# Kernel tuning notes

Hardware: AMD Instinct MI355X
Metric: run time of the kernel (lower is better)

Reference implementation:

```python
import jax, jax.numpy as jnp
import numpy as np

EPS = 1e-5  # torch BatchNorm2d default


def _signature_depth3(path):
    """Truncated (depth-3) path signature via Chen's relation.
    path: [B, P, ch] (P points). Returns [B, ch + ch^2 + ch^3] in signatory
    layout (level 1, then row-major flattened levels 2 and 3)."""
    dx = path[:, 1:] - path[:, :-1]  # [B, P-1, ch] increments
    B, _, ch = dx.shape

    def step(carry, v):
        s1, s2, s3 = carry  # [B,ch], [B,ch,ch], [B,ch,ch,ch]
        vv = v[:, :, None] * v[:, None, :]          # v (x) v
        e2 = 0.5 * vv                               # v^(x)2 / 2!
        e3 = vv[:, :, :, None] * v[:, None, None, :] / 6.0  # v^(x)3 / 3!
        n1 = s1 + v
        n2 = s2 + s1[:, :, None] * v[:, None, :] + e2
        n3 = (s3
              + s2[:, :, :, None] * v[:, None, None, :]
              + s1[:, :, None, None] * e2[:, None, :, :]
              + e3)
        return (n1, n2, n3), None

    init = (jnp.zeros((B, ch), dx.dtype),
            jnp.zeros((B, ch, ch), dx.dtype),
            jnp.zeros((B, ch, ch, ch), dx.dtype))
    (s1, s2, s3), _ = jax.lax.scan(step, init, jnp.transpose(dx, (1, 0, 2)))
    return jnp.concatenate([s1, s2.reshape(B, -1), s3.reshape(B, -1)], axis=1)


def setup_inputs() -> dict:
    key = jax.random.key(0)
    ks = jax.random.split(key, 5)
    N, C, J, T, L = 16, 64, 25, 128, 9
    sic, out_dim = 8, 64
    ch = sic + 1                      # +1 time channel
    sig_ch = ch + ch**2 + ch**3       # 819
    x = jax.random.normal(ks[0], (N, C, J, T, L), jnp.float32)
    conv_w = jax.random.normal(ks[1], (sic, C), jnp.float32) * 0.1
    conv_b = jax.random.normal(ks[2], (sic,), jnp.float32) * 0.1
    bn_gamma = jnp.ones((sic,), jnp.float32)
    bn_beta = jnp.zeros((sic,), jnp.float32)
    lin_w = jax.random.normal(ks[3], (out_dim, sig_ch), jnp.float32) * 0.03
    lin_b = jax.random.normal(ks[4], (out_dim,), jnp.float32) * 0.03
    return dict(x=x, conv_w=conv_w, conv_b=conv_b, bn_gamma=bn_gamma,
                bn_beta=bn_beta, lin_w=lin_w, lin_b=lin_b)


def reference(x, conv_w, conv_b, bn_gamma, bn_beta, lin_w, lin_b):
    N, C, J, T, L = x.shape
    # 1x1 conv over channel dim (applied to [N*L, C, J, T] in torch, which is
    # the same per-position linear map)
    y = jnp.einsum('ncjtl,oc->nojtl', x, conv_w) + conv_b[None, :, None, None, None]
    y = jax.nn.relu(y)
    # BatchNorm2d (training mode): stats over all dims except channel
    mean = y.mean(axis=(0, 2, 3, 4), keepdims=True)
    var = ((y - mean) ** 2).mean(axis=(0, 2, 3, 4), keepdims=True)
    y = ((y - mean) * jax.lax.rsqrt(var + EPS)
         * bn_gamma[None, :, None, None, None] + bn_beta[None, :, None, None, None])
    # -> [N*J*T, L, sic] stream per (n, joint, frame)
    B = N * J * T
    p = jnp.transpose(y, (0, 2, 3, 4, 1)).reshape(B, L, -1)
    # signatory.Augment(include_time=True): prepend time channel in [0, 1]
    t = jnp.broadcast_to(jnp.linspace(0.0, 1.0, L, dtype=x.dtype)[None, :, None], (B, L, 1))
    p = jnp.concatenate([t, p], axis=-1)  # [B, L, ch]
    # signature(..., basepoint=True): prepend zero point
    path = jnp.concatenate([jnp.zeros((B, 1, p.shape[-1]), p.dtype), p], axis=1)
    sig = _signature_depth3(path)          # [B, 819]
    z = sig @ lin_w.T + lin_b              # [B, out_dim]
    return jnp.transpose(z.reshape(N, J, T, -1), (0, 3, 1, 2))  # [N, C, J, T]
```

## Files before the change

kernel.cpp:

```cpp
#include <hip/hip_runtime.h>
#include <hip/hip_bf16.h>

typedef unsigned short u16;
typedef __attribute__((ext_vector_type(8))) short short8;
typedef __attribute__((ext_vector_type(4))) float f32x4;

#define N_    16
#define C_    64
#define J_    25
#define T_    128
#define L_    9
#define SIC   8
#define OUT_  64
#define BTOT  (N_*J_*T_)
#define CNT   (BTOT*L_)
#define KPAD  896
#define SPB   28

#define K1_BLOCKS 512
#define K1_ACT    225

#define PART_OFF  0
#define PART2_OFF 16384
#define SS_OFF    32768
#define BT_OFF    40960
#define Y_OFF     69632
#define WS_NEED   ((size_t)(Y_OFF + BTOT*72) * 4)

__device__ __forceinline__ short to_bf16(float x) {
  union { __hip_bfloat16 h; u16 u; } cv;
  cv.h = __float2bfloat16(x);
  return (short)cv.u;
}

__global__ __launch_bounds__(256) void k1_conv(
    const float* __restrict__ x, const float* __restrict__ cw,
    const float* __restrict__ cb, float* __restrict__ yws,
    float* __restrict__ part) {
  __shared__ float wl[SIC * C_];
  __shared__ float bl[SIC];
  __shared__ float wsum[4][16];
  int tid = threadIdx.x;
  wl[tid] = cw[tid];
  wl[tid + 256] = cw[tid + 256];
  if (tid < SIC) bl[tid] = cb[tid];
  __syncthreads();

  float vals[16];
#pragma unroll
  for (int q = 0; q < 16; q++) vals[q] = 0.f;

  if (tid < K1_ACT) {
    int p0 = (blockIdx.x * K1_ACT + tid) * 4;
    int n = p0 / 28800, rem = p0 % 28800;
    int jj = rem / 1152, tl0 = rem % 1152;
    const float* xp = x + (size_t)(n * 1600 + jj) * 1152 + tl0;

    float acc[4][8];
#pragma unroll
    for (int p = 0; p < 4; p++)
#pragma unroll
      for (int o = 0; o < 8; o++) acc[p][o] = bl[o];

#pragma unroll 8
    for (int c = 0; c < C_; c++) {
      float4 xv = *(const float4*)(xp + (size_t)c * 28800);
#pragma unroll
      for (int o = 0; o < 8; o++) {
        float wv = wl[o * C_ + c];
        acc[0][o] = fmaf(xv.x, wv, acc[0][o]);
        acc[1][o] = fmaf(xv.y, wv, acc[1][o]);
        acc[2][o] = fmaf(xv.z, wv, acc[2][o]);
        acc[3][o] = fmaf(xv.w, wv, acc[3][o]);
      }
    }
    float4* dst = (float4*)(yws + (size_t)p0 * 8);
#pragma unroll
    for (int p = 0; p < 4; p++) {
#pragma unroll
      for (int o = 0; o < 8; o++) acc[p][o] = fmaxf(acc[p][o], 0.f);
      dst[p * 2]     = make_float4(acc[p][0], acc[p][1], acc[p][2], acc[p][3]);
      dst[p * 2 + 1] = make_float4(acc[p][4], acc[p][5], acc[p][6], acc[p][7]);
#pragma unroll
      for (int o = 0; o < 8; o++) {
        vals[o] += acc[p][o];
        vals[8 + o] += acc[p][o] * acc[p][o];
      }
    }
  }

  int lane = tid & 63, wid = tid >> 6;
#pragma unroll
  for (int v = 0; v < 16; v++) {
    float s = vals[v];
    for (int off = 32; off > 0; off >>= 1) s += __shfl_down(s, off, 64);
    if (lane == 0) wsum[wid][v] = s;
  }
  __syncthreads();
  if (tid < 16)
    part[blockIdx.x * 16 + tid] = wsum[0][tid] + wsum[1][tid] + wsum[2][tid] + wsum[3][tid];
}

__global__ __launch_bounds__(256) void k2_red1(
    const float* __restrict__ part, float* __restrict__ part2) {
  __shared__ float red[16][16];
  int tid = threadIdx.x;
  int val = tid & 15, grp = tid >> 4;
  red[grp][val] = part[(blockIdx.x * 16 + grp) * 16 + val];
  __syncthreads();
  if (tid < 16) {
    float tot = 0.f;
#pragma unroll
    for (int g = 0; g < 16; g++) tot += red[g][tid];
    part2[blockIdx.x * 16 + tid] = tot;
  }
}

__global__ __launch_bounds__(256) void k2_stats2(
    const float* __restrict__ part2, const float* __restrict__ gamma,
    const float* __restrict__ beta, float* __restrict__ ss) {
  __shared__ float red[16][16];
  int tid = threadIdx.x;
  int val = tid & 15, grp = tid >> 4;
  red[grp][val] = part2[grp * 16 + val] + part2[(grp + 16) * 16 + val];
  __syncthreads();
  if (tid < 16) {
    float tot = 0.f;
#pragma unroll
    for (int g = 0; g < 16; g++) tot += red[g][tid];
    red[0][tid] = tot;
  }
  __syncthreads();
  if (tid < 8) {
    float mean = red[0][tid] * (1.f / CNT);
    float var  = red[0][8 + tid] * (1.f / CNT) - mean * mean;
    float sc = gamma[tid] * rsqrtf(var + 1e-5f);
    ss[tid] = sc;
    ss[8 + tid] = beta[tid] - mean * sc;
  }
}

__global__ __launch_bounds__(256) void k2_bt(
    const float* __restrict__ lw, u16* __restrict__ Bt) {
  int idx = blockIdx.x * 256 + threadIdx.x;
  if (idx >= OUT_ * KPAD) return;
  int o = idx / KPAD, k = idx % KPAD;
  float v = 0.f;
  if (k < 864) {
    int i = k / 96, p = k % 96;
    if (p < 91) {
      int orig = (p == 0) ? i : (p < 10 ? 9 + i * 9 + (p - 1) : 90 + i * 81 + (p - 10));
      v = lw[o * 819 + orig];
    }
  }
  Bt[idx] = (u16)to_bf16(v);
}

__global__ __launch_bounds__(256, 2) void k3_fused(
    const float* __restrict__ yws, const float* __restrict__ ss,
    const u16* __restrict__ Bt, const float* __restrict__ lb,
    float* __restrict__ out) {
  __shared__ __align__(16) u16 sig_lds[32 * KPAD];
  __shared__ __align__(16) float ylds[SPB * 72];
  __shared__ float ssl[16];
  __shared__ float lbl[64];
  int tid = threadIdx.x;
  if (tid < 16) ssl[tid] = ss[tid];
  if (tid >= 64 && tid < 128) lbl[tid - 64] = lb[tid - 64];
  int gBase = blockIdx.x * SPB;
  int valid = BTOT - gBase; if (valid > SPB) valid = SPB;
  __syncthreads();

  if (tid < SPB * 9) {
    int s = tid / 9;
    if (s < valid) {
      const float4* src = (const float4*)(yws + (size_t)gBase * 72 + (size_t)tid * 8);
      float4 a = src[0], b = src[1];
      float* drow = ylds + tid * 8;
      drow[0] = fmaf(a.x, ssl[0], ssl[8]);
      drow[1] = fmaf(a.y, ssl[1], ssl[9]);
      drow[2] = fmaf(a.z, ssl[2], ssl[10]);
      drow[3] = fmaf(a.w, ssl[3], ssl[11]);
      drow[4] = fmaf(b.x, ssl[4], ssl[12]);
      drow[5] = fmaf(b.y, ssl[5], ssl[13]);
      drow[6] = fmaf(b.z, ssl[6], ssl[14]);
      drow[7] = fmaf(b.w, ssl[7], ssl[15]);
    }
  }
  __syncthreads();

  int s = tid / 9, i = tid % 9;
  bool act = (tid < SPB * 9) && (s < valid);
  if (act) {
    const float* yrow = ylds + s * 72;
    int i1 = (i == 0) ? 0 : (i - 1);
    float s1 = 0.f, s2[9], s3[81], prev[8], prevvi = 0.f;
#pragma unroll
    for (int jj = 0; jj < 9; jj++) s2[jj] = 0.f;
#pragma unroll
    for (int q = 0; q < 81; q++) s3[q] = 0.f;
#pragma unroll
    for (int c = 0; c < 8; c++) prev[c] = 0.f;

#pragma unroll 3
    for (int l = 0; l < 9; l++) {
      float4 a4 = *(const float4*)(yrow + l * 8);
      float4 b4 = *(const float4*)(yrow + l * 8 + 4);
      float ldsv = yrow[l * 8 + i1];
      float cur[8] = {a4.x, a4.y, a4.z, a4.w, b4.x, b4.y, b4.z, b4.w};
      float v[9];
      v[0] = (l == 0) ? 0.f : 0.125f;
#pragma unroll
      for (int c = 0; c < 8; c++) v[c + 1] = cur[c] - prev[c];
      float curvi = (i == 0) ? (float)l * 0.125f : ldsv;
      float vi = curvi - prevvi;
      prevvi = curvi;
      float aa = fmaf(vi, (1.f / 6.f), 0.5f * s1);
      float b2 = fmaf(vi, 0.5f, s1);
#pragma unroll
      for (int jj = 0; jj < 9; jj++) {
        float tj = fmaf(aa, v[jj], s2[jj]);
#pragma unroll
        for (int k = 0; k < 9; k++) s3[jj * 9 + k] = fmaf(tj, v[k], s3[jj * 9 + k]);
        s2[jj] = fmaf(b2, v[jj], s2[jj]);
      }
      s1 += vi;
#pragma unroll
      for (int c = 0; c < 8; c++) prev[c] = cur[c];
    }

    u16* rowbase = sig_lds + s * KPAD;
    int sw = s & 7;
    {
      short8 ch;
      ch[0] = to_bf16(s1);
#pragma unroll
      for (int w = 0; w < 7; w++) ch[w + 1] = to_bf16(s2[w]);
      *(short8*)&rowbase[(((i * 12 + 0) ^ sw) * 8)] = ch;
    }
    {
      short8 ch;
      ch[0] = to_bf16(s2[7]); ch[1] = to_bf16(s2[8]);
#pragma unroll
      for (int w = 0; w < 6; w++) ch[w + 2] = to_bf16(s3[w]);
      *(short8*)&rowbase[(((i * 12 + 1) ^ sw) * 8)] = ch;
    }
#pragma unroll
    for (int c = 2; c <= 10; c++) {
      short8 ch;
#pragma unroll
      for (int w = 0; w < 8; w++) ch[w] = to_bf16(s3[c * 8 - 10 + w]);
      *(short8*)&rowbase[(((i * 12 + c) ^ sw) * 8)] = ch;
    }
    {
      short8 ch;
      ch[0] = to_bf16(s3[78]); ch[1] = to_bf16(s3[79]); ch[2] = to_bf16(s3[80]);
      ch[3] = 0; ch[4] = 0; ch[5] = 0; ch[6] = 0; ch[7] = 0;
      *(short8*)&rowbase[(((i * 12 + 11) ^ sw) * 8)] = ch;
    }
    if (i < 4) {
      short8 z = {0, 0, 0, 0, 0, 0, 0, 0};
      *(short8*)&rowbase[(((108 + i) ^ sw) * 8)] = z;
    }
  }
  {
    short8 z = {0, 0, 0, 0, 0, 0, 0, 0};
    int padChunks = (32 - valid) * 112;
    for (int e = tid; e < padChunks; e += 256) {
      int r = valid + e / 112, sl = e % 112;
      *(short8*)&sig_lds[r * KPAD + sl * 8] = z;
    }
  }
  __syncthreads();

  int w = tid >> 6, l = tid & 63;
  int brow = (w << 4) + (l & 15);
  const short8* bp = (const short8*)(Bt + (size_t)brow * KPAD);
  int arow0 = (l & 15), arow1 = 16 + (l & 15);
  int asw = arow0 & 7;
  f32x4 acc0 = {0, 0, 0, 0}, acc1 = {0, 0, 0, 0};
#pragma unroll
  for (int ks = 0; ks < 28; ks++) {
    int s4 = ks * 4 + (l >> 4);
    short8 bfrag = bp[s4];
    short8 a0 = *(const short8*)&sig_lds[arow0 * KPAD + ((s4 ^ asw) * 8)];
    short8 a1 = *(const short8*)&sig_lds[arow1 * KPAD + ((s4 ^ asw) * 8)];
    acc0 = __builtin_amdgcn_mfma_f32_16x16x32_bf16(a0, bfrag, acc0, 0, 0, 0);
    acc1 = __builtin_amdgcn_mfma_f32_16x16x32_bf16(a1, bfrag, acc1, 0, 0, 0);
  }
  __syncthreads();

  float* c_lds = (float*)sig_lds;
  int o = (w << 4) + (l & 15);
#pragma unroll
  for (int r = 0; r < 4; r++) {
    int m0 = (l >> 4) * 4 + r;
    c_lds[o * 33 + m0] = acc0[r];
    c_lds[o * 33 + 16 + m0] = acc1[r];
  }
  __syncthreads();
  for (int e = tid; e < 2048; e += 256) {
    int o2 = e >> 5, m = e & 31;
    if (m < valid) {
      int b = gBase + m;
      int n = b / (J_ * T_), rem = b % (J_ * T_);
      int j = rem >> 7, t = rem & (T_ - 1);
      out[(((size_t)n * OUT_ + o2) * J_ + j) * T_ + t] = c_lds[o2 * 33 + m] + lbl[o2];
    }
  }
}

extern "C" void kernel_launch(void* const* d_in, const int* in_sizes, int n_in,
                              void* d_out, int out_size, void* d_ws, size_t ws_size,
                              hipStream_t stream) {
  const float* x     = (const float*)d_in[0];
  const float* cw    = (const float*)d_in[1];
  const float* cb    = (const float*)d_in[2];
  const float* gamma = (const float*)d_in[3];
  const float* beta  = (const float*)d_in[4];
  const float* lw    = (const float*)d_in[5];
  const float* lbias = (const float*)d_in[6];
  float* out = (float*)d_out;
  float* ws  = (float*)d_ws;
  if (ws_size < WS_NEED) return;

  float* part  = ws + PART_OFF;
  float* part2 = ws + PART2_OFF;
  float* ss    = ws + SS_OFF;
  u16*   bt    = (u16*)(ws + BT_OFF);
  float* yws   = ws + Y_OFF;

  hipLaunchKernelGGL(k2_bt, dim3((OUT_ * KPAD + 255) / 256), dim3(256), 0, stream, lw, bt);
  hipLaunchKernelGGL(k1_conv, dim3(K1_BLOCKS), dim3(256), 0, stream, x, cw, cb, yws, part);
  hipLaunchKernelGGL(k2_red1, dim3(32), dim3(256), 0, stream, part, part2);
  hipLaunchKernelGGL(k2_stats2, dim3(1), dim3(256), 0, stream, part2, gamma, beta, ss);

  int nblk3 = (BTOT + SPB - 1) / SPB;
  hipLaunchKernelGGL(k3_fused, dim3(nblk3), dim3(256), 0, stream, yws, ss, bt, lbias, out);
}
```

Measured before the change: 81.46 us.

## Merge weight prep into conv, collapse stats reduction, shrink LDS for occupancy

Folds the bf16 weight-transposition kernel into the conv kernel as extra blocks and merges the two stat-reduction kernels into one, cutting the launch count from five to three. The conv kernel now gives each thread two positions instead of four and uses all 256 threads, with transposed weights in LDS so they load as vectors. The fused signature kernel aliases the normalized-input staging buffer onto the signature LDS tile, uses 29 rows instead of 32, and skips the last K step, allowing three blocks per CU. This adds an extra barrier before signature writes and clamps out-of-range MFMA rows, which increases register pressure under the new launch bound.

Measured after the change: 70.82 us. 13.1% less time.

```diff
diff --git a/kernel.cpp b/kernel.cpp
--- a/kernel.cpp
+++ b/kernel.cpp
@@ -15,16 +15,17 @@
 #define BTOT  (N_*J_*T_)
 #define CNT   (BTOT*L_)
 #define KPAD  896
+#define NKS   27
 #define SPB   28
 
-#define K1_BLOCKS 512
-#define K1_ACT    225
+#define K1C_BLOCKS 900
+#define K1BT_BLOCKS 224
+#define BT_ELEMS (OUT_*KPAD)
 
 #define PART_OFF  0
-#define PART2_OFF 16384
-#define SS_OFF    32768
-#define BT_OFF    40960
-#define Y_OFF     69632
+#define SS_OFF    16384
+#define BT_OFF    32768
+#define Y_OFF     65536
 #define WS_NEED   ((size_t)(Y_OFF + BTOT*72) * 4)
 
 __device__ __forceinline__ short to_bf16(float x) {
@@ -35,57 +36,75 @@
 
 __global__ __launch_bounds__(256) void k1_conv(
     const float* __restrict__ x, const float* __restrict__ cw,
-    const float* __restrict__ cb, float* __restrict__ yws,
-    float* __restrict__ part) {
-  __shared__ float wl[SIC * C_];
+    const float* __restrict__ cb, const float* __restrict__ lw,
+    float* __restrict__ yws, float* __restrict__ part, u16* __restrict__ Bt) {
+  int tid = threadIdx.x;
+
+  if (blockIdx.x >= K1C_BLOCKS) {
+    int idx = (blockIdx.x - K1C_BLOCKS) * 256 + tid;
+    if (idx < BT_ELEMS) {
+      int o = idx / KPAD, k = idx % KPAD;
+      float v = 0.f;
+      if (k < 864) {
+        int i = k / 96, p = k % 96;
+        if (p < 91) {
+          int orig = (p == 0) ? i : (p < 10 ? 9 + i * 9 + (p - 1) : 90 + i * 81 + (p - 10));
+          v = lw[o * 819 + orig];
+        }
+      }
+      Bt[idx] = (u16)to_bf16(v);
+    }
+    return;
+  }
+
+  __shared__ float wlT[C_ * SIC];
   __shared__ float bl[SIC];
   __shared__ float wsum[4][16];
-  int tid = threadIdx.x;
-  wl[tid] = cw[tid];
-  wl[tid + 256] = cw[tid + 256];
+  wlT[tid] = cw[(tid & 7) * C_ + (tid >> 3)];
+  wlT[tid + 256] = cw[(tid & 7) * C_ + ((tid + 256) >> 3)];
   if (tid < SIC) bl[tid] = cb[tid];
   __syncthreads();
 
+  int p0 = (blockIdx.x * 256 + tid) * 2;
+  int n = p0 / 28800, rem = p0 % 28800;
+  int jj = rem / 1152, tl0 = rem % 1152;
+  const float* xp = x + (size_t)(n * 1600 + jj) * 1152 + tl0;
+
+  float acc[2][8];
+#pragma unroll
+  for (int p = 0; p < 2; p++)
+#pragma unroll
+    for (int o = 0; o < 8; o++) acc[p][o] = bl[o];
+
+#pragma unroll 8
+  for (int c = 0; c < C_; c++) {
+    float2 xv = *(const float2*)(xp + (size_t)c * 28800);
+    float4 w0 = *(const float4*)&wlT[c * 8];
+    float4 w1 = *(const float4*)&wlT[c * 8 + 4];
+    acc[0][0] = fmaf(xv.x, w0.x, acc[0][0]); acc[1][0] = fmaf(xv.y, w0.x, acc[1][0]);
+    acc[0][1] = fmaf(xv.x, w0.y, acc[0][1]); acc[1][1] = fmaf(xv.y, w0.y, acc[1][1]);
+    acc[0][2] = fmaf(xv.x, w0.z, acc[0][2]); acc[1][2] = fmaf(xv.y, w0.z, acc[1][2]);
+    acc[0][3] = fmaf(xv.x, w0.w, acc[0][3]); acc[1][3] = fmaf(xv.y, w0.w, acc[1][3]);
+    acc[0][4] = fmaf(xv.x, w1.x, acc[0][4]); acc[1][4] = fmaf(xv.y, w1.x, acc[1][4]);
+    acc[0][5] = fmaf(xv.x, w1.y, acc[0][5]); acc[1][5] = fmaf(xv.y, w1.y, acc[1][5]);
+    acc[0][6] = fmaf(xv.x, w1.z, acc[0][6]); acc[1][6] = fmaf(xv.y, w1.z, acc[1][6]);
+    acc[0][7] = fmaf(xv.x, w1.w, acc[0][7]); acc[1][7] = fmaf(xv.y, w1.w, acc[1][7]);
+  }
+
   float vals[16];
 #pragma unroll
   for (int q = 0; q < 16; q++) vals[q] = 0.f;
-
-  if (tid < K1_ACT) {
-    int p0 = (blockIdx.x * K1_ACT + tid) * 4;
-    int n = p0 / 28800, rem = p0 % 28800;
-    int jj = rem / 1152, tl0 = rem % 1152;
-    const float* xp = x + (size_t)(n * 1600 + jj) * 1152 + tl0;
-
-    float acc[4][8];
-#pragma unroll
-    for (int p = 0; p < 4; p++)
-#pragma unroll
-      for (int o = 0; o < 8; o++) acc[p][o] = bl[o];
-
-#pragma unroll 8
-    for (int c = 0; c < C_; c++) {
-      float4 xv = *(const float4*)(xp + (size_t)c * 28800);
-#pragma unroll
-      for (int o = 0; o < 8; o++) {
-        float wv = wl[o * C_ + c];
-        acc[0][o] = fmaf(xv.x, wv, acc[0][o]);
-        acc[1][o] = fmaf(xv.y, wv, acc[1][o]);
-        acc[2][o] = fmaf(xv.z, wv, acc[2][o]);
-        acc[3][o] = fmaf(xv.w, wv, acc[3][o]);
-      }
-    }
-    float4* dst = (float4*)(yws + (size_t)p0 * 8);
-#pragma unroll
-    for (int p = 0; p < 4; p++) {
-#pragma unroll
-      for (int o = 0; o < 8; o++) acc[p][o] = fmaxf(acc[p][o], 0.f);
-      dst[p * 2]     = make_float4(acc[p][0], acc[p][1], acc[p][2], acc[p][3]);
-      dst[p * 2 + 1] = make_float4(acc[p][4], acc[p][5], acc[p][6], acc[p][7]);
-#pragma unroll
-      for (int o = 0; o < 8; o++) {
-        vals[o] += acc[p][o];
-        vals[8 + o] += acc[p][o] * acc[p][o];
-      }
+  float4* dst = (float4*)(yws + (size_t)p0 * 8);
+#pragma unroll
+  for (int p = 0; p < 2; p++) {
+#pragma unroll
+    for (int o = 0; o < 8; o++) acc[p][o] = fmaxf(acc[p][o], 0.f);
+    dst[p * 2]     = make_float4(acc[p][0], acc[p][1], acc[p][2], acc[p][3]);
+    dst[p * 2 + 1] = make_float4(acc[p][4], acc[p][5], acc[p][6], acc[p][7]);
+#pragma unroll
+    for (int o = 0; o < 8; o++) {
+      vals[o] += acc[p][o];
+      vals[8 + o] += acc[p][o] * acc[p][o];
     }
   }
 
@@ -101,28 +120,22 @@
     part[blockIdx.x * 16 + tid] = wsum[0][tid] + wsum[1][tid] + wsum[2][tid] + wsum[3][tid];
 }
 
-__global__ __launch_bounds__(256) void k2_red1(
-    const float* __restrict__ part, float* __restrict__ part2) {
-  __shared__ float red[16][16];
-  int tid = threadIdx.x;
-  int val = tid & 15, grp = tid >> 4;
-  red[grp][val] = part[(blockIdx.x * 16 + grp) * 16 + val];
-  __syncthreads();
-  if (tid < 16) {
-    float tot = 0.f;
-#pragma unroll
-    for (int g = 0; g < 16; g++) tot += red[g][tid];
-    part2[blockIdx.x * 16 + tid] = tot;
-  }
-}
-
-__global__ __launch_bounds__(256) void k2_stats2(
-    const float* __restrict__ part2, const float* __restrict__ gamma,
+__global__ __launch_bounds__(256) void k2_stats(
+    const float* __restrict__ part, const float* __restrict__ gamma,
     const float* __restrict__ beta, float* __restrict__ ss) {
   __shared__ float red[16][16];
   int tid = threadIdx.x;
   int val = tid & 15, grp = tid >> 4;
-  red[grp][val] = part2[grp * 16 + val] + part2[(grp + 16) * 16 + val];
+  float s0 = 0.f, s1 = 0.f, s2 = 0.f, s3 = 0.f;
+  int b = grp;
+  for (; b + 48 < K1C_BLOCKS; b += 64) {
+    s0 += part[b * 16 + val];
+    s1 += part[(b + 16) * 16 + val];
+    s2 += part[(b + 32) * 16 + val];
+    s3 += part[(b + 48) * 16 + val];
+  }
+  for (; b < K1C_BLOCKS; b += 16) s0 += part[b * 16 + val];
+  red[grp][val] = (s0 + s1) + (s2 + s3);
   __syncthreads();
   if (tid < 16) {
     float tot = 0.f;
@@ -140,30 +153,14 @@
   }
 }
 
-__global__ __launch_bounds__(256) void k2_bt(
-    const float* __restrict__ lw, u16* __restrict__ Bt) {
-  int idx = blockIdx.x * 256 + threadIdx.x;
-  if (idx >= OUT_ * KPAD) return;
-  int o = idx / KPAD, k = idx % KPAD;
-  float v = 0.f;
-  if (k < 864) {
-    int i = k / 96, p = k % 96;
-    if (p < 91) {
-      int orig = (p == 0) ? i : (p < 10 ? 9 + i * 9 + (p - 1) : 90 + i * 81 + (p - 10));
-      v = lw[o * 819 + orig];
-    }
-  }
-  Bt[idx] = (u16)to_bf16(v);
-}
-
-__global__ __launch_bounds__(256, 2) void k3_fused(
+__global__ __launch_bounds__(256, 3) void k3_fused(
     const float* __restrict__ yws, const float* __restrict__ ss,
     const u16* __restrict__ Bt, const float* __restrict__ lb,
     float* __restrict__ out) {
-  __shared__ __align__(16) u16 sig_lds[32 * KPAD];
-  __shared__ __align__(16) float ylds[SPB * 72];
+  __shared__ __align__(16) u16 sig_lds[29 * KPAD];
   __shared__ float ssl[16];
   __shared__ float lbl[64];
+  float* ylds = (float*)sig_lds;
   int tid = threadIdx.x;
   if (tid < 16) ssl[tid] = ss[tid];
   if (tid >= 64 && tid < 128) lbl[tid - 64] = lb[tid - 64];
@@ -187,18 +184,27 @@
       drow[7] = fmaf(b.w, ssl[7], ssl[15]);
     }
   }
+  {
+    short8 z = {0, 0, 0, 0, 0, 0, 0, 0};
+    int padChunks = (29 - valid) * 112;
+    for (int e = tid; e < padChunks; e += 256) {
+      int r = valid + e / 112, sl = e % 112;
+      *(short8*)&sig_lds[r * KPAD + sl * 8] = z;
+    }
+  }
   __syncthreads();
 
   int s = tid / 9, i = tid % 9;
   bool act = (tid < SPB * 9) && (s < valid);
+  float s1 = 0.f, s2[9], s3[81];
+#pragma unroll
+  for (int jj = 0; jj < 9; jj++) s2[jj] = 0.f;
+#pragma unroll
+  for (int q = 0; q < 81; q++) s3[q] = 0.f;
   if (act) {
     const float* yrow = ylds + s * 72;
     int i1 = (i == 0) ? 0 : (i - 1);
-    float s1 = 0.f, s2[9], s3[81], prev[8], prevvi = 0.f;
-#pragma unroll
-    for (int jj = 0; jj < 9; jj++) s2[jj] = 0.f;
-#pragma unroll
-    for (int q = 0; q < 81; q++) s3[q] = 0.f;
+    float prev[8], prevvi = 0.f;
 #pragma unroll
     for (int c = 0; c < 8; c++) prev[c] = 0.f;
 
@@ -228,7 +234,10 @@
 #pragma unroll
       for (int c = 0; c < 8; c++) prev[c] = cur[c];
     }
-
+  }
+  __syncthreads();
+
+  if (act) {
     u16* rowbase = sig_lds + s * KPAD;
     int sw = s & 7;
     {
@@ -258,33 +267,22 @@
       ch[3] = 0; ch[4] = 0; ch[5] = 0; ch[6] = 0; ch[7] = 0;
       *(short8*)&rowbase[(((i * 12 + 11) ^ sw) * 8)] = ch;
     }
-    if (i < 4) {
-      short8 z = {0, 0, 0, 0, 0, 0, 0, 0};
-      *(short8*)&rowbase[(((108 + i) ^ sw) * 8)] = z;
-    }
-  }
-  {
-    short8 z = {0, 0, 0, 0, 0, 0, 0, 0};
-    int padChunks = (32 - valid) * 112;
-    for (int e = tid; e < padChunks; e += 256) {
-      int r = valid + e / 112, sl = e % 112;
-      *(short8*)&sig_lds[r * KPAD + sl * 8] = z;
-    }
   }
   __syncthreads();
 
   int w = tid >> 6, l = tid & 63;
   int brow = (w << 4) + (l & 15);
   const short8* bp = (const short8*)(Bt + (size_t)brow * KPAD);
-  int arow0 = (l & 15), arow1 = 16 + (l & 15);
-  int asw = arow0 & 7;
+  int arow0 = (l & 15);
+  int arow1 = 16 + (l & 15); if (arow1 > 28) arow1 = 28;
+  int asw0 = arow0 & 7, asw1 = arow1 & 7;
   f32x4 acc0 = {0, 0, 0, 0}, acc1 = {0, 0, 0, 0};
 #pragma unroll
-  for (int ks = 0; ks < 28; ks++) {
+  for (int ks = 0; ks < NKS; ks++) {
     int s4 = ks * 4 + (l >> 4);
     short8 bfrag = bp[s4];
-    short8 a0 = *(const short8*)&sig_lds[arow0 * KPAD + ((s4 ^ asw) * 8)];
-    short8 a1 = *(const short8*)&sig_lds[arow1 * KPAD + ((s4 ^ asw) * 8)];
+    short8 a0 = *(const short8*)&sig_lds[arow0 * KPAD + ((s4 ^ asw0) * 8)];
+    short8 a1 = *(const short8*)&sig_lds[arow1 * KPAD + ((s4 ^ asw1) * 8)];
     acc0 = __builtin_amdgcn_mfma_f32_16x16x32_bf16(a0, bfrag, acc0, 0, 0, 0);
     acc1 = __builtin_amdgcn_mfma_f32_16x16x32_bf16(a1, bfrag, acc1, 0, 0, 0);
   }
@@ -324,16 +322,14 @@
   float* ws  = (float*)d_ws;
   if (ws_size < WS_NEED) return;
 
-  float* part  = ws + PART_OFF;
-  float* part2 = ws + PART2_OFF;
-  float* ss    = ws + SS_OFF;
-  u16*   bt    = (u16*)(ws + BT_OFF);
-  float* yws   = ws + Y_OFF;
-
-  hipLaunchKernelGGL(k2_bt, dim3((OUT_ * KPAD + 255) / 256), dim3(256), 0, stream, lw, bt);
-  hipLaunchKernelGGL(k1_conv, dim3(K1_BLOCKS), dim3(256), 0, stream, x, cw, cb, yws, part);
-  hipLaunchKernelGGL(k2_red1, dim3(32), dim3(256), 0, stream, part, part2);
-  hipLaunchKernelGGL(k2_stats2, dim3(1), dim3(256), 0, stream, part2, gamma, beta, ss);
+  float* part = ws + PART_OFF;
+  float* ss   = ws + SS_OFF;
+  u16*   bt   = (u16*)(ws + BT_OFF);
+  float* yws  = ws + Y_OFF;
+
+  hipLaunchKernelGGL(k1_conv, dim3(K1C_BLOCKS + K1BT_BLOCKS), dim3(256), 0, stream,
+                     x, cw, cb, lw, yws, part, bt);
+  hipLaunchKernelGGL(k2_stats, dim3(1), dim3(256), 0, stream, part, gamma, beta, ss);
 
   int nblk3 = (BTOT + SPB - 1) / SPB;
   hipLaunchKernelGGL(k3_fused, dim3(nblk3), dim3(256), 0, stream, yws, ss, bt, lbias, out);
```
